# Kernel tuning notes

Hardware: AMD Instinct MI355X
Metric: run time of the kernel (lower is better)

The kernel has to match this reference:

```python
import jax, jax.numpy as jnp
import numpy as np

B, C, H_IMG, W_IMG = 16, 384, 56, 56
NUM_HEADS = 6
HEAD_DIM = C // NUM_HEADS
BN_EPS = 1e-5


def _bn(x, gamma, beta, mean, var):
    # x: [b, ch, n] or [b, ch, h, w]; per-channel affine normalization (eval-mode BatchNorm)
    shape = (1, -1) + (1,) * (x.ndim - 2)
    scale = (gamma / jnp.sqrt(var + BN_EPS)).reshape(shape)
    shift = (beta - mean * gamma / jnp.sqrt(var + BN_EPS)).reshape(shape)
    return x * scale + shift


def setup_inputs() -> dict:
    key = jax.random.key(0)
    ks = jax.random.split(key, 12)
    c2 = 2 * C
    return {
        "x": jax.random.normal(ks[0], (B, C, H_IMG, W_IMG), jnp.float32),
        "qk_w": jax.random.normal(ks[1], (c2, C // 2), jnp.float32) * 0.05,
        "qk_gamma": jax.random.uniform(ks[2], (c2,), jnp.float32, 0.5, 1.5),
        "qk_beta": jax.random.normal(ks[3], (c2,), jnp.float32) * 0.1,
        "qk_mean": jax.random.normal(ks[4], (c2,), jnp.float32) * 0.1,
        "qk_var": jax.random.uniform(ks[5], (c2,), jnp.float32, 0.5, 1.5),
        "pe_w": jax.random.normal(ks[6], (C, 1, 3, 3), jnp.float32) * 0.1,
        "pe_gamma": jax.random.uniform(ks[7], (C,), jnp.float32, 0.5, 1.5),
        "pe_beta": jax.random.normal(ks[8], (C,), jnp.float32) * 0.1,
        "pe_mean": jax.random.normal(ks[9], (C,), jnp.float32) * 0.1,
        "pe_var": jax.random.uniform(ks[10], (C,), jnp.float32, 0.5, 1.5),
    }


def reference(x, qk_w, qk_gamma, qk_beta, qk_mean, qk_var,
              pe_w, pe_gamma, pe_beta, pe_mean, pe_var):
    b, c, h, w = x.shape
    n = h * w
    s = n ** (-0.5)
    nh, hd = NUM_HEADS, HEAD_DIM

    # grouped (groups=2) 1x1 conv: out channels [0:c] from input [0:c/2], [c:2c] from [c/2:c]
    xg = x.reshape(b, 2, c // 2, n)                       # [b, 2, c/2, n]
    wg = qk_w.reshape(2, c, c // 2)                       # [group, out_per_group, in_per_group]
    qk = jnp.einsum('bgin,goi->bgon', xg, wg).reshape(b, 2 * c, n)
    qk = _bn(qk, qk_gamma, qk_beta, qk_mean, qk_var)
    qk = jax.nn.elu(qk) + 1.0

    qk = qk.reshape(b, 2, nh, hd, n)
    q, k = qk[:, 0], qk[:, 1]                             # [b, H, d, n]
    v = x.reshape(b, nh, hd, n)                           # [b, H, d, n]

    # kv = (k*s) @ (v^T * s): [b, H, d, d]
    kv = jnp.einsum('bhdn,bhen->bhde', k * s, v * s)
    # numerator: q^T @ kv -> [b, H, n, d]
    num = jnp.einsum('bhdn,bhde->bhne', q, kv)
    # denominator: q^T @ mean_n(k) -> [b, H, n]
    den = jnp.einsum('bhdn,bhd->bhn', q, k.mean(axis=-1)) + 1e-6
    attn = (num / den[..., None]).transpose(0, 1, 3, 2).reshape(b, c, h, w)

    # depthwise 3x3 conv positional encoding on v (= x) + BN
    pe = jax.lax.conv_general_dilated(
        x, pe_w, window_strides=(1, 1), padding=((1, 1), (1, 1)),
        feature_group_count=c, dimension_numbers=('NCHW', 'OIHW', 'NCHW'))
    pe = _bn(pe, pe_gamma, pe_beta, pe_mean, pe_var)

    return attn + pe
```

## Files before the change

### kernel.cpp

```cpp
#include <hip/hip_runtime.h>
#include <math.h>

#define N_SP 3136
#define BN_EPS 1e-5f

typedef __attribute__((ext_vector_type(8))) short short8;
typedef __attribute__((ext_vector_type(4))) float f32x4;

#define QK_SZ   (16*2*384*N_SP)
#define KVP_OFF (QK_SZ)
#define KVP_SZ  (16*6*7*64*80)
#define KV_OFF  (KVP_OFF + KVP_SZ)
#define KV_SZ   (16*6*64*64)
#define KM_OFF  (KV_OFF + KV_SZ)
#define KM_SZ   (16*6*64)
#define WH_OFF  (KM_OFF + KM_SZ)
#define WSPLIT_N (2*384*192)

__device__ __forceinline__ void bsplit(float f, ushort& h, ushort& l) {
    uint u = __float_as_uint(f);
    uint hr = (u + 0x7FFFu + ((u >> 16) & 1u)) >> 16;
    h = (ushort)hr;
    float fh = __uint_as_float(hr << 16);
    float fl = f - fh;
    uint v = __float_as_uint(fl);
    l = (ushort)((v + 0x7FFFu + ((v >> 16) & 1u)) >> 16);
}

__global__ __launch_bounds__(256) void p0_wsplit(
    const float* __restrict__ qk_w, ushort* __restrict__ wh, ushort* __restrict__ wl)
{
    int idx = blockIdx.x * 256 + threadIdx.x;
    if (idx >= WSPLIT_N) return;
    ushort h, l;
    bsplit(qk_w[idx], h, l);
    wh[idx] = h;
    wl[idx] = l;
}

__global__ __launch_bounds__(256) void k1_qk_mfma(
    const float* __restrict__ x, const ushort* __restrict__ wh, const ushort* __restrict__ wl,
    const float* __restrict__ gamma, const float* __restrict__ beta,
    const float* __restrict__ mean, const float* __restrict__ var,
    float* __restrict__ qk_out)
{
    __shared__ __align__(16) ushort Ah[8192];
    __shared__ __align__(16) ushort Al[8192];
    __shared__ __align__(16) ushort Bh[4096];
    __shared__ __align__(16) ushort Bl[4096];

    const int bx = blockIdx.x;
    const int by = blockIdx.y;
    const int bz = blockIdx.z;
    const int b = bz >> 1, gg = bz & 1;
    const int t = threadIdx.x;
    const int lane = t & 63, wv = t >> 6;
    const int wr = wv >> 1, wc = wv & 1;
    const int lg = lane >> 4, l15 = lane & 15;

    f32x4 acc[4][2];
    #pragma unroll
    for (int m = 0; m < 4; ++m)
        #pragma unroll
        for (int nf = 0; nf < 2; ++nf)
            acc[m][nf] = (f32x4){0.f, 0.f, 0.f, 0.f};

    const float* xg = x + (size_t)(b * 384 + gg * 192) * N_SP + bx * 64;
    const ushort* whg = wh + (gg * 384 + by * 128) * 192;
    const ushort* wlg = wl + (gg * 384 + by * 128) * 192;

    for (int kt = 0; kt < 3; ++kt) {
        #pragma unroll
        for (int li = 0; li < 4; ++li) {
            int c = li * 256 + t;
            int row = c >> 3, kb = c & 7;
            int goff = row * 192 + kt * 64 + kb * 8;
            float4 vh = *(const float4*)(whg + goff);
            float4 vl = *(const float4*)(wlg + goff);
            int ch = (row * 8 + (kb ^ (row & 7))) * 8;
            *(float4*)&Ah[ch] = vh;
            *(float4*)&Al[ch] = vl;
        }
        #pragma unroll
        for (int li = 0; li < 2; ++li) {
            int idx = li * 256 + t;
            int kp = idx >> 4;
            int nq = idx & 15;
            int k0 = kp * 2;
            const float* px = xg + (size_t)(kt * 64 + k0) * N_SP + nq * 4;
            float4 v0 = *(const float4*)px;
            float4 v1 = *(const float4*)(px + N_SP);
            ushort h0[4], l0[4], h1[4], l1[4];
            float a0[4] = {v0.x, v0.y, v0.z, v0.w};
            float a1[4] = {v1.x, v1.y, v1.z, v1.w};
            #pragma unroll
            for (int i = 0; i < 4; ++i) { bsplit(a0[i], h0[i], l0[i]); bsplit(a1[i], h1[i], l1[i]); }
            int kb = k0 >> 3, ks = (k0 & 6) >> 1;
            #pragma unroll
            for (int i = 0; i < 4; ++i) {
                int n = nq * 4 + i;
                int chunk = n * 8 + (kb ^ ((n >> 1) & 7));
                ((uint*)Bh)[chunk * 4 + ks] = (uint)h0[i] | ((uint)h1[i] << 16);
                ((uint*)Bl)[chunk * 4 + ks] = (uint)l0[i] | ((uint)l1[i] << 16);
            }
        }
        __syncthreads();
        #pragma unroll
        for (int s = 0; s < 2; ++s) {
            short8 ah[4], al[4], bh[2], bl[2];
            int kb = s * 4 + lg;
            #pragma unroll
            for (int m = 0; m < 4; ++m) {
                int row = wr * 64 + m * 16 + l15;
                int ch = (row * 8 + (kb ^ (row & 7))) * 8;
                ah[m] = *(const short8*)&Ah[ch];
                al[m] = *(const short8*)&Al[ch];
            }
            #pragma unroll
            for (int nf = 0; nf < 2; ++nf) {
                int n = wc * 32 + nf * 16 + l15;
                int ch = (n * 8 + (kb ^ ((n >> 1) & 7))) * 8;
                bh[nf] = *(const short8*)&Bh[ch];
                bl[nf] = *(const short8*)&Bl[ch];
            }
            #pragma unroll
            for (int m = 0; m < 4; ++m)
                #pragma unroll
                for (int nf = 0; nf < 2; ++nf) {
                    acc[m][nf] = __builtin_amdgcn_mfma_f32_16x16x32_bf16(ah[m], bh[nf], acc[m][nf], 0, 0, 0);
                    acc[m][nf] = __builtin_amdgcn_mfma_f32_16x16x32_bf16(ah[m], bl[nf], acc[m][nf], 0, 0, 0);
                    acc[m][nf] = __builtin_amdgcn_mfma_f32_16x16x32_bf16(al[m], bh[nf], acc[m][nf], 0, 0, 0);
                }
        }
        __syncthreads();
    }

    float* scs = (float*)Bh;
    float* shs = scs + 128;
    if (t < 128) {
        int ch = gg * 384 + by * 128 + t;
        float sc = gamma[ch] / sqrtf(var[ch] + BN_EPS);
        scs[t] = sc;
        shs[t] = beta[ch] - mean[ch] * sc;
    }
    __syncthreads();

    size_t obase = ((size_t)(b * 2 + gg) * 384 + by * 128) * N_SP + bx * 64 + wc * 32;
    #pragma unroll
    for (int m = 0; m < 4; ++m)
        #pragma unroll
        for (int nf = 0; nf < 2; ++nf) {
            #pragma unroll
            for (int r = 0; r < 4; ++r) {
                int orow = wr * 64 + m * 16 + lg * 4 + r;
                float v = acc[m][nf][r] * scs[orow] + shs[orow];
                v = v > 0.f ? v + 1.f : __expf(v);
                qk_out[obase + (size_t)orow * N_SP + nf * 16 + l15] = v;
            }
        }
}

__global__ __launch_bounds__(256) void k2_kv_mfma(
    const float* __restrict__ x, const float* __restrict__ qk,
    float* __restrict__ kv_part)
{
    __shared__ __align__(16) ushort Kh[4096], Kl[4096];
    __shared__ __align__(16) ushort Vh[5120], Vl[5120];

    const int chunk = blockIdx.x;
    const int h = blockIdx.y, b = blockIdx.z;
    const int t = threadIdx.x;
    const int lane = t & 63, wv = t >> 6;
    const int lg = lane >> 4, l15 = lane & 15;

    const float* kp = qk + (size_t)((b*2+1)*384 + h*64) * N_SP;
    const float* vp = x  + (size_t)(b*384 + h*64) * N_SP;

    #pragma unroll
    for (int li = 0; li < 4; ++li) {
        int idx = li * 256 + t;
        int row = 64 + (idx >> 6), col = idx & 63;
        int off = (row * 8 + ((col >> 3) ^ (row & 7))) * 8 + (col & 7);
        Vh[off] = (row == 64) ? (ushort)0x3F80 : (ushort)0;
        Vl[off] = 0;
    }

    f32x4 acc[5];
    #pragma unroll
    for (int nf = 0; nf < 5; ++nf) acc[nf] = (f32x4){0.f, 0.f, 0.f, 0.f};

    for (int sub = 0; sub < 7; ++sub) {
        int n0 = chunk * 448 + sub * 64;
        #pragma unroll
        for (int li = 0; li < 4; ++li) {
            int idx = li * 256 + t;
            int row = idx >> 4, sc = idx & 15;
            int off = (row * 8 + ((sc >> 1) ^ (row & 7))) * 8 + (sc & 1) * 4;
            float4 kf = *(const float4*)&kp[(size_t)row * N_SP + n0 + sc * 4];
            ushort h0,h1,h2,h3,l0,l1,l2,l3;
            bsplit(kf.x,h0,l0); bsplit(kf.y,h1,l1); bsplit(kf.z,h2,l2); bsplit(kf.w,h3,l3);
            ((uint*)&Kh[off])[0] = (uint)h0 | ((uint)h1 << 16);
            ((uint*)&Kh[off])[1] = (uint)h2 | ((uint)h3 << 16);
            ((uint*)&Kl[off])[0] = (uint)l0 | ((uint)l1 << 16);
            ((uint*)&Kl[off])[1] = (uint)l2 | ((uint)l3 << 16);
            float4 vf = *(const float4*)&vp[(size_t)row * N_SP + n0 + sc * 4];
            bsplit(vf.x,h0,l0); bsplit(vf.y,h1,l1); bsplit(vf.z,h2,l2); bsplit(vf.w,h3,l3);
            ((uint*)&Vh[off])[0] = (uint)h0 | ((uint)h1 << 16);
            ((uint*)&Vh[off])[1] = (uint)h2 | ((uint)h3 << 16);
            ((uint*)&Vl[off])[0] = (uint)l0 | ((uint)l1 << 16);
            ((uint*)&Vl[off])[1] = (uint)l2 | ((uint)l3 << 16);
        }
        __syncthreads();
        #pragma unroll
        for (int s = 0; s < 2; ++s) {
            int arow = wv * 16 + l15;
            int akb = (s * 4 + lg) ^ (arow & 7);
            short8 ah = *(const short8*)&Kh[(arow * 8 + akb) * 8];
            short8 al = *(const short8*)&Kl[(arow * 8 + akb) * 8];
            #pragma unroll
            for (int nf = 0; nf < 5; ++nf) {
                int brow = nf * 16 + l15;
                int bkb = (s * 4 + lg) ^ (brow & 7);
                short8 bh = *(const short8*)&Vh[(brow * 8 + bkb) * 8];
                short8 bl = *(const short8*)&Vl[(brow * 8 + bkb) * 8];
                acc[nf] = __builtin_amdgcn_mfma_f32_16x16x32_bf16(ah, bh, acc[nf], 0, 0, 0);
                acc[nf] = __builtin_amdgcn_mfma_f32_16x16x32_bf16(ah, bl, acc[nf], 0, 0, 0);
                acc[nf] = __builtin_amdgcn_mfma_f32_16x16x32_bf16(al, bh, acc[nf], 0, 0, 0);
            }
        }
        __syncthreads();
    }

    size_t base = (size_t)((b*6 + h)*7 + chunk) * 64 * 80;
    #pragma unroll
    for (int nf = 0; nf < 5; ++nf)
        #pragma unroll
        for (int r = 0; r < 4; ++r) {
            int d = wv * 16 + lg * 4 + r;
            kv_part[base + (size_t)d * 80 + nf * 16 + l15] = acc[nf][r];
        }
}

__global__ __launch_bounds__(256) void k2b_reduce(
    const float* __restrict__ kv_part,
    float* __restrict__ kv, float* __restrict__ km)
{
    int idx = blockIdx.x*256 + threadIdx.x;
    const float inv_n = 1.0f / (float)N_SP;
    if (idx < 16*6*64*64) {
        int bh = idx >> 12, de = idx & 4095;
        int d = de >> 6, e = de & 63;
        float s = 0.f;
        #pragma unroll
        for (int c = 0; c < 7; ++c) s += kv_part[((size_t)(bh*7+c)*64 + d)*80 + e];
        kv[idx] = s * inv_n;
    }
    if (idx < 16*6*64) {
        int bh = idx >> 6, d = idx & 63;
        float s = 0.f;
        #pragma unroll
        for (int c = 0; c < 7; ++c) s += kv_part[((size_t)(bh*7+c)*64 + d)*80 + 64];
        km[idx] = s * inv_n;
    }
}

__global__ __launch_bounds__(256) void k3_attn_pe(
    const float* __restrict__ x, const float* __restrict__ qk,
    const float* __restrict__ kv, const float* __restrict__ km,
    const float* __restrict__ pw,
    const float* __restrict__ pgamma, const float* __restrict__ pbeta,
    const float* __restrict__ pmean, const float* __restrict__ pvar,
    float* __restrict__ out)
{
    __shared__ float qs[64][68];
    __shared__ float kms[64];
    const int bx = blockIdx.x;
    const int h = blockIdx.y, b = blockIdx.z;
    const int t = threadIdx.x, tx = t & 15, ty = t >> 4;
    const int n0 = bx*64;
    const float* qp  = qk + (size_t)((b*2+0)*384 + h*64)*N_SP;
    const float* kvp = kv + (b*6+h)*4096;
    #pragma unroll
    for (int l = 0; l < 4; ++l) {
        int idx = t + l*256;
        int d = idx >> 4, c = idx & 15;
        *(float4*)&qs[d][c*4] = *(const float4*)&qp[(size_t)d*N_SP + n0 + c*4];
    }
    if (t < 64) kms[t] = km[(b*6+h)*64 + t];
    __syncthreads();

    float acc[4][4] = {};
    float den[4] = {};
    #pragma unroll 8
    for (int d = 0; d < 64; ++d) {
        float4 qn = *(const float4*)&qs[d][tx*4];
        float4 ke = *(const float4*)&kvp[d*64 + ty*4];
        float qq[4] = {qn.x,qn.y,qn.z,qn.w}, kk[4] = {ke.x,ke.y,ke.z,ke.w};
        float kmd = kms[d];
        #pragma unroll
        for (int p = 0; p < 4; ++p) {
            den[p] += qq[p]*kmd;
            #pragma unroll
            for (int j = 0; j < 4; ++j) acc[p][j] += qq[p]*kk[j];
        }
    }

    const int p0 = n0 + tx*4;
    const int y = p0 / 56, xc = p0 % 56;
    #pragma unroll
    for (int j = 0; j < 4; ++j) {
        int c = h*64 + ty*4 + j;
        const float* xp = x + ((size_t)b*384 + c)*N_SP;
        float s6[3][6];
        #pragma unroll
        for (int dy = 0; dy < 3; ++dy) {
            int yy = y + dy - 1;
            bool yok = (yy >= 0) && (yy < 56);
            float4 mid = make_float4(0.f,0.f,0.f,0.f);
            float lf = 0.f, rt = 0.f;
            if (yok) {
                const float* xr = xp + yy*56;
                mid = *(const float4*)&xr[xc];
                if (xc > 0)  lf = xr[xc-1];
                if (xc < 52) rt = xr[xc+4];
            }
            s6[dy][0]=lf; s6[dy][1]=mid.x; s6[dy][2]=mid.y;
            s6[dy][3]=mid.z; s6[dy][4]=mid.w; s6[dy][5]=rt;
        }
        float w9[9];
        #pragma unroll
        for (int q = 0; q < 9; ++q) w9[q] = pw[c*9 + q];
        float sc2 = pgamma[c] / sqrtf(pvar[c] + BN_EPS);
        float sh2 = pbeta[c] - pmean[c]*sc2;
        float4 r;
        float* pr = (float*)&r;
        #pragma unroll
        for (int p = 0; p < 4; ++p) {
            float conv = 0.f;
            #pragma unroll
            for (int dy = 0; dy < 3; ++dy)
                #pragma unroll
                for (int dx = 0; dx < 3; ++dx)
                    conv += w9[dy*3+dx] * s6[dy][p + dx];
            pr[p] = acc[p][j] / (den[p] + 1e-6f) + (conv*sc2 + sh2);
        }
        *(float4*)&out[((size_t)b*384 + c)*N_SP + p0] = r;
    }
}

extern "C" void kernel_launch(void* const* d_in, const int* in_sizes, int n_in,
                              void* d_out, int out_size, void* d_ws, size_t ws_size,
                              hipStream_t stream)
{
    const float* x        = (const float*)d_in[0];
    const float* qk_w     = (const float*)d_in[1];
    const float* qk_gamma = (const float*)d_in[2];
    const float* qk_beta  = (const float*)d_in[3];
    const float* qk_mean  = (const float*)d_in[4];
    const float* qk_var   = (const float*)d_in[5];
    const float* pe_w     = (const float*)d_in[6];
    const float* pe_gamma = (const float*)d_in[7];
    const float* pe_beta  = (const float*)d_in[8];
    const float* pe_mean  = (const float*)d_in[9];
    const float* pe_var   = (const float*)d_in[10];
    float* out = (float*)d_out;

    float* ws      = (float*)d_ws;
    float* qk      = ws;
    float* kv_part = ws + KVP_OFF;
    float* kv      = ws + KV_OFF;
    float* km      = ws + KM_OFF;
    ushort* whp    = (ushort*)(ws + WH_OFF);
    ushort* wlp    = whp + WSPLIT_N;

    hipLaunchKernelGGL(p0_wsplit, dim3((WSPLIT_N + 255)/256), dim3(256), 0, stream,
                       qk_w, whp, wlp);
    dim3 g1(49, 3, 32);
    hipLaunchKernelGGL(k1_qk_mfma, g1, dim3(256), 0, stream,
                       x, whp, wlp, qk_gamma, qk_beta, qk_mean, qk_var, qk);
    dim3 g2(7, 6, 16);
    hipLaunchKernelGGL(k2_kv_mfma, g2, dim3(256), 0, stream, x, qk, kv_part);
    hipLaunchKernelGGL(k2b_reduce, dim3(1536), dim3(256), 0, stream,
                       kv_part, kv, km);
    dim3 g3(49, 6, 16);
    hipLaunchKernelGGL(k3_attn_pe, g3, dim3(256), 0, stream,
                       x, qk, kv, km, pe_w, pe_gamma, pe_beta, pe_mean, pe_var, out);
}
```

Before: 219.8 us.

## Compute attention numerator and denominator in k3 via split-bf16 MFMA

The reduce kernel now emits kv and the k-mean row, transposed and split into bf16 high/low halves, padded to 80 rows. The attention kernel converts its q tile to split bf16 in swizzled shared memory. It then computes numerator and denominator with three-pass MFMA instead of scalar FMAs, staging the results through shared memory for the PE epilogue. This cuts the per-block FP32 FMA work in k3, at the cost of extra conversion, shared memory traffic, two more barriers, and slight precision change from bf16x3 emulation.

```diff
diff --git a/kernel.cpp b/kernel.cpp
--- a/kernel.cpp
+++ b/kernel.cpp
@@ -10,11 +10,9 @@
 #define QK_SZ   (16*2*384*N_SP)
 #define KVP_OFF (QK_SZ)
 #define KVP_SZ  (16*6*7*64*80)
-#define KV_OFF  (KVP_OFF + KVP_SZ)
-#define KV_SZ   (16*6*64*64)
-#define KM_OFF  (KV_OFF + KV_SZ)
-#define KM_SZ   (16*6*64)
-#define WH_OFF  (KM_OFF + KM_SZ)
+#define KVT_OFF (KVP_OFF + KVP_SZ)
+#define KVT_FSZ (2*96*80*64/2)
+#define WH_OFF  (KVT_OFF + KVT_FSZ)
 #define WSPLIT_N (2*384*192)
 
 __device__ __forceinline__ void bsplit(float f, ushort& h, ushort& l) {
@@ -243,95 +241,146 @@
 
 __global__ __launch_bounds__(256) void k2b_reduce(
     const float* __restrict__ kv_part,
-    float* __restrict__ kv, float* __restrict__ km)
-{
-    int idx = blockIdx.x*256 + threadIdx.x;
+    ushort* __restrict__ kvt_h, ushort* __restrict__ kvt_l)
+{
+    const int bh = blockIdx.x;
+    const int t = threadIdx.x;
     const float inv_n = 1.0f / (float)N_SP;
-    if (idx < 16*6*64*64) {
-        int bh = idx >> 12, de = idx & 4095;
-        int d = de >> 6, e = de & 63;
+    const float* base = kv_part + (size_t)bh * 7 * 64 * 80;
+    ushort* oh = kvt_h + (size_t)bh * 80 * 64;
+    ushort* ol = kvt_l + (size_t)bh * 80 * 64;
+    for (int i = t; i < 80 * 64; i += 256) {
+        int e = i >> 6, d = i & 63;
         float s = 0.f;
-        #pragma unroll
-        for (int c = 0; c < 7; ++c) s += kv_part[((size_t)(bh*7+c)*64 + d)*80 + e];
-        kv[idx] = s * inv_n;
-    }
-    if (idx < 16*6*64) {
-        int bh = idx >> 6, d = idx & 63;
-        float s = 0.f;
-        #pragma unroll
-        for (int c = 0; c < 7; ++c) s += kv_part[((size_t)(bh*7+c)*64 + d)*80 + 64];
-        km[idx] = s * inv_n;
-    }
-}
-
+        if (e <= 64) {
+            #pragma unroll
+            for (int c = 0; c < 7; ++c) s += base[(size_t)(c * 64 + d) * 80 + e];
+            s *= inv_n;
+        }
+        ushort h, l;
+        bsplit(s, h, l);
+        oh[i] = h; ol[i] = l;
+    }
+}
+
+#define ATT_STRIDE 68
 __global__ __launch_bounds__(256) void k3_attn_pe(
     const float* __restrict__ x, const float* __restrict__ qk,
-    const float* __restrict__ kv, const float* __restrict__ km,
+    const ushort* __restrict__ kvt_h, const ushort* __restrict__ kvt_l,
     const float* __restrict__ pw,
     const float* __restrict__ pgamma, const float* __restrict__ pbeta,
     const float* __restrict__ pmean, const float* __restrict__ pvar,
     float* __restrict__ out)
 {
-    __shared__ float qs[64][68];
-    __shared__ float kms[64];
+    __shared__ __align__(16) float SBF[ATT_STRIDE * 64 + 64];
+    ushort* Qh = (ushort*)SBF;
+    ushort* Ql = Qh + 4096;
+
     const int bx = blockIdx.x;
     const int h = blockIdx.y, b = blockIdx.z;
-    const int t = threadIdx.x, tx = t & 15, ty = t >> 4;
-    const int n0 = bx*64;
-    const float* qp  = qk + (size_t)((b*2+0)*384 + h*64)*N_SP;
-    const float* kvp = kv + (b*6+h)*4096;
-    #pragma unroll
-    for (int l = 0; l < 4; ++l) {
-        int idx = t + l*256;
-        int d = idx >> 4, c = idx & 15;
-        *(float4*)&qs[d][c*4] = *(const float4*)&qp[(size_t)d*N_SP + n0 + c*4];
-    }
-    if (t < 64) kms[t] = km[(b*6+h)*64 + t];
+    const int t = threadIdx.x;
+    const int lane = t & 63, wv = t >> 6;
+    const int lg = lane >> 4, l15 = lane & 15;
+    const int n0 = bx * 64;
+    const float* qp = qk + (size_t)((b*2+0)*384 + h*64) * N_SP + n0;
+
+    #pragma unroll
+    for (int li = 0; li < 2; ++li) {
+        int idx = li * 256 + t;
+        int kp2 = idx >> 4;
+        int nq = idx & 15;
+        int k0 = kp2 * 2;
+        const float* px = qp + (size_t)k0 * N_SP + nq * 4;
+        float4 v0 = *(const float4*)px;
+        float4 v1 = *(const float4*)(px + N_SP);
+        ushort h0[4], l0[4], h1[4], l1[4];
+        float a0[4] = {v0.x, v0.y, v0.z, v0.w};
+        float a1[4] = {v1.x, v1.y, v1.z, v1.w};
+        #pragma unroll
+        for (int i = 0; i < 4; ++i) { bsplit(a0[i], h0[i], l0[i]); bsplit(a1[i], h1[i], l1[i]); }
+        int kb = k0 >> 3, ks = (k0 & 6) >> 1;
+        #pragma unroll
+        for (int i = 0; i < 4; ++i) {
+            int n = nq * 4 + i;
+            int chunk = n * 8 + (kb ^ ((n >> 1) & 7));
+            ((uint*)Qh)[chunk * 4 + ks] = (uint)h0[i] | ((uint)h1[i] << 16);
+            ((uint*)Ql)[chunk * 4 + ks] = (uint)l0[i] | ((uint)l1[i] << 16);
+        }
+    }
     __syncthreads();
 
-    float acc[4][4] = {};
-    float den[4] = {};
-    #pragma unroll 8
-    for (int d = 0; d < 64; ++d) {
-        float4 qn = *(const float4*)&qs[d][tx*4];
-        float4 ke = *(const float4*)&kvp[d*64 + ty*4];
-        float qq[4] = {qn.x,qn.y,qn.z,qn.w}, kk[4] = {ke.x,ke.y,ke.z,ke.w};
-        float kmd = kms[d];
-        #pragma unroll
-        for (int p = 0; p < 4; ++p) {
-            den[p] += qq[p]*kmd;
-            #pragma unroll
-            for (int j = 0; j < 4; ++j) acc[p][j] += qq[p]*kk[j];
-        }
-    }
-
-    const int p0 = n0 + tx*4;
+    short8 bqh[2], bql[2];
+    #pragma unroll
+    for (int s = 0; s < 2; ++s) {
+        int n = wv * 16 + l15;
+        int chunk = n * 8 + ((s * 4 + lg) ^ ((n >> 1) & 7));
+        bqh[s] = *(const short8*)&Qh[chunk * 8];
+        bql[s] = *(const short8*)&Ql[chunk * 8];
+    }
+    __syncthreads();
+
+    const ushort* ahb = kvt_h + (size_t)(b*6 + h) * 80 * 64;
+    const ushort* alb = kvt_l + (size_t)(b*6 + h) * 80 * 64;
+    f32x4 acc[5];
+    #pragma unroll
+    for (int m = 0; m < 5; ++m) acc[m] = (f32x4){0.f, 0.f, 0.f, 0.f};
+    #pragma unroll
+    for (int s = 0; s < 2; ++s) {
+        #pragma unroll
+        for (int m = 0; m < 5; ++m) {
+            int off = (m * 16 + l15) * 64 + (s * 4 + lg) * 8;
+            short8 ah = *(const short8*)&ahb[off];
+            short8 al = *(const short8*)&alb[off];
+            acc[m] = __builtin_amdgcn_mfma_f32_16x16x32_bf16(ah, bqh[s], acc[m], 0, 0, 0);
+            acc[m] = __builtin_amdgcn_mfma_f32_16x16x32_bf16(ah, bql[s], acc[m], 0, 0, 0);
+            acc[m] = __builtin_amdgcn_mfma_f32_16x16x32_bf16(al, bqh[s], acc[m], 0, 0, 0);
+        }
+    }
+
+    {
+        int ncol = wv * 16 + l15;
+        #pragma unroll
+        for (int m = 0; m < 4; ++m)
+            #pragma unroll
+            for (int r = 0; r < 4; ++r)
+                SBF[(m * 16 + lg * 4 + r) * ATT_STRIDE + ncol] = acc[m][r];
+        if (lg == 0)
+            SBF[ATT_STRIDE * 64 + ncol] = acc[4][0];
+    }
+    __syncthreads();
+
+    const int tx = t & 15, ty = t >> 4;
+    const int p0 = n0 + tx * 4;
     const int y = p0 / 56, xc = p0 % 56;
+    float den[4];
+    #pragma unroll
+    for (int p = 0; p < 4; ++p) den[p] = SBF[ATT_STRIDE * 64 + tx * 4 + p] + 1e-6f;
     #pragma unroll
     for (int j = 0; j < 4; ++j) {
-        int c = h*64 + ty*4 + j;
-        const float* xp = x + ((size_t)b*384 + c)*N_SP;
+        int cc = ty * 4 + j;
+        int c = h * 64 + cc;
+        const float* xp = x + ((size_t)b * 384 + c) * N_SP;
         float s6[3][6];
         #pragma unroll
         for (int dy = 0; dy < 3; ++dy) {
             int yy = y + dy - 1;
             bool yok = (yy >= 0) && (yy < 56);
-            float4 mid = make_float4(0.f,0.f,0.f,0.f);
+            float4 mid = make_float4(0.f, 0.f, 0.f, 0.f);
             float lf = 0.f, rt = 0.f;
             if (yok) {
-                const float* xr = xp + yy*56;
+                const float* xr = xp + yy * 56;
                 mid = *(const float4*)&xr[xc];
-                if (xc > 0)  lf = xr[xc-1];
-                if (xc < 52) rt = xr[xc+4];
-            }
-            s6[dy][0]=lf; s6[dy][1]=mid.x; s6[dy][2]=mid.y;
-            s6[dy][3]=mid.z; s6[dy][4]=mid.w; s6[dy][5]=rt;
+                if (xc > 0)  lf = xr[xc - 1];
+                if (xc < 52) rt = xr[xc + 4];
+            }
+            s6[dy][0] = lf;  s6[dy][1] = mid.x; s6[dy][2] = mid.y;
+            s6[dy][3] = mid.z; s6[dy][4] = mid.w; s6[dy][5] = rt;
         }
         float w9[9];
         #pragma unroll
-        for (int q = 0; q < 9; ++q) w9[q] = pw[c*9 + q];
+        for (int q = 0; q < 9; ++q) w9[q] = pw[c * 9 + q];
         float sc2 = pgamma[c] / sqrtf(pvar[c] + BN_EPS);
-        float sh2 = pbeta[c] - pmean[c]*sc2;
+        float sh2 = pbeta[c] - pmean[c] * sc2;
         float4 r;
         float* pr = (float*)&r;
         #pragma unroll
@@ -341,10 +390,11 @@
             for (int dy = 0; dy < 3; ++dy)
                 #pragma unroll
                 for (int dx = 0; dx < 3; ++dx)
-                    conv += w9[dy*3+dx] * s6[dy][p + dx];
-            pr[p] = acc[p][j] / (den[p] + 1e-6f) + (conv*sc2 + sh2);
-        }
-        *(float4*)&out[((size_t)b*384 + c)*N_SP + p0] = r;
+                    conv += w9[dy * 3 + dx] * s6[dy][p + dx];
+            float num = SBF[cc * ATT_STRIDE + tx * 4 + p];
+            pr[p] = num / den[p] + (conv * sc2 + sh2);
+        }
+        *(float4*)&out[((size_t)b * 384 + c) * N_SP + p0] = r;
     }
 }
 
@@ -368,8 +418,8 @@
     float* ws      = (float*)d_ws;
     float* qk      = ws;
     float* kv_part = ws + KVP_OFF;
-    float* kv      = ws + KV_OFF;
-    float* km      = ws + KM_OFF;
+    ushort* kvt_h  = (ushort*)(ws + KVT_OFF);
+    ushort* kvt_l  = kvt_h + 96 * 80 * 64;
     ushort* whp    = (ushort*)(ws + WH_OFF);
     ushort* wlp    = whp + WSPLIT_N;
 
@@ -380,9 +430,9 @@
                        x, whp, wlp, qk_gamma, qk_beta, qk_mean, qk_var, qk);
     dim3 g2(7, 6, 16);
     hipLaunchKernelGGL(k2_kv_mfma, g2, dim3(256), 0, stream, x, qk, kv_part);
-    hipLaunchKernelGGL(k2b_reduce, dim3(1536), dim3(256), 0, stream,
-                       kv_part, kv, km);
+    hipLaunchKernelGGL(k2b_reduce, dim3(96), dim3(256), 0, stream,
+                       kv_part, kvt_h, kvt_l);
     dim3 g3(49, 6, 16);
     hipLaunchKernelGGL(k3_attn_pe, g3, dim3(256), 0, stream,
-                       x, qk, kv, km, pe_w, pe_gamma, pe_beta, pe_mean, pe_var, out);
-}
+                       x, qk, kvt_h, kvt_l, pe_w, pe_gamma, pe_beta, pe_mean, pe_var, out);
+}
```

Measured after the change: 240.5 us. +9.4%, slower.

## Pre-split K to bf16 pairs, fold PE BN into weights, restructure attention kernel

Applied to the files above, without the earlier changes.

In k1 the K half is now stored as packed bf16 hi/lo pairs, so k2 no longer re-splits K; Q is written to its own fp32 buffer. The PE BatchNorm scale is folded into the depthwise weights in the prep kernel. The kv reduction is reorganised per (b,h) block. The final kernel maps one pixel per lane and 16 channels per wave, reading q straight from global memory instead of staging it in LDS, and does the 3x3 conv with scalar loads. The LDS swizzle for B in k1 also changes. The new conv path issues more scattered scalar loads of x, and the attention loop relies on the cache for q reuse.

```diff
diff --git a/kernel.cpp b/kernel.cpp
--- a/kernel.cpp
+++ b/kernel.cpp
@@ -7,15 +7,21 @@
 typedef __attribute__((ext_vector_type(8))) short short8;
 typedef __attribute__((ext_vector_type(4))) float f32x4;
 
-#define QK_SZ   (16*2*384*N_SP)
-#define KVP_OFF (QK_SZ)
+#define K_SZ    (16*384*N_SP)
+#define QB_OFF  (K_SZ)
+#define QB_SZ   (16*384*N_SP)
+#define KVP_OFF (QB_OFF + QB_SZ)
 #define KVP_SZ  (16*6*7*64*80)
-#define KV_OFF  (KVP_OFF + KVP_SZ)
-#define KV_SZ   (16*6*64*64)
-#define KM_OFF  (KV_OFF + KV_SZ)
+#define KVF_OFF (KVP_OFF + KVP_SZ)
+#define KVF_SZ  (16*6*64*64)
+#define KM_OFF  (KVF_OFF + KVF_SZ)
 #define KM_SZ   (16*6*64)
 #define WH_OFF  (KM_OFF + KM_SZ)
 #define WSPLIT_N (2*384*192)
+#define PWS_OFF (WH_OFF + WSPLIT_N)
+#define PSH_OFF (PWS_OFF + 384*9)
+
+#define FSWZ(n) ((((n) >> 1) ^ ((n) >> 2)) & 7)
 
 __device__ __forceinline__ void bsplit(float f, ushort& h, ushort& l) {
     uint u = __float_as_uint(f);
@@ -27,22 +33,33 @@
     l = (ushort)((v + 0x7FFFu + ((v >> 16) & 1u)) >> 16);
 }
 
-__global__ __launch_bounds__(256) void p0_wsplit(
-    const float* __restrict__ qk_w, ushort* __restrict__ wh, ushort* __restrict__ wl)
+__global__ __launch_bounds__(256) void p0_prep(
+    const float* __restrict__ qk_w, const float* __restrict__ pe_w,
+    const float* __restrict__ pgamma, const float* __restrict__ pbeta,
+    const float* __restrict__ pmean, const float* __restrict__ pvar,
+    ushort* __restrict__ wh, ushort* __restrict__ wl,
+    float* __restrict__ pwsc, float* __restrict__ psh)
 {
     int idx = blockIdx.x * 256 + threadIdx.x;
-    if (idx >= WSPLIT_N) return;
-    ushort h, l;
-    bsplit(qk_w[idx], h, l);
-    wh[idx] = h;
-    wl[idx] = l;
+    if (idx < WSPLIT_N) {
+        ushort h, l;
+        bsplit(qk_w[idx], h, l);
+        wh[idx] = h;
+        wl[idx] = l;
+    }
+    if (idx < 384) {
+        float sc = pgamma[idx] / sqrtf(pvar[idx] + BN_EPS);
+        psh[idx] = pbeta[idx] - pmean[idx] * sc;
+        #pragma unroll
+        for (int q = 0; q < 9; ++q) pwsc[idx * 9 + q] = pe_w[idx * 9 + q] * sc;
+    }
 }
 
 __global__ __launch_bounds__(256) void k1_qk_mfma(
     const float* __restrict__ x, const ushort* __restrict__ wh, const ushort* __restrict__ wl,
     const float* __restrict__ gamma, const float* __restrict__ beta,
     const float* __restrict__ mean, const float* __restrict__ var,
-    float* __restrict__ qk_out)
+    uint* __restrict__ kq, float* __restrict__ qbuf)
 {
     __shared__ __align__(16) ushort Ah[8192];
     __shared__ __align__(16) ushort Al[8192];
@@ -99,7 +116,7 @@
             #pragma unroll
             for (int i = 0; i < 4; ++i) {
                 int n = nq * 4 + i;
-                int chunk = n * 8 + (kb ^ ((n >> 1) & 7));
+                int chunk = n * 8 + (kb ^ FSWZ(n));
                 ((uint*)Bh)[chunk * 4 + ks] = (uint)h0[i] | ((uint)h1[i] << 16);
                 ((uint*)Bl)[chunk * 4 + ks] = (uint)l0[i] | ((uint)l1[i] << 16);
             }
@@ -119,7 +136,7 @@
             #pragma unroll
             for (int nf = 0; nf < 2; ++nf) {
                 int n = wc * 32 + nf * 16 + l15;
-                int ch = (n * 8 + (kb ^ ((n >> 1) & 7))) * 8;
+                int ch = (n * 8 + (kb ^ FSWZ(n))) * 8;
                 bh[nf] = *(const short8*)&Bh[ch];
                 bl[nf] = *(const short8*)&Bl[ch];
             }
@@ -145,23 +162,40 @@
     }
     __syncthreads();
 
-    size_t obase = ((size_t)(b * 2 + gg) * 384 + by * 128) * N_SP + bx * 64 + wc * 32;
-    #pragma unroll
-    for (int m = 0; m < 4; ++m)
-        #pragma unroll
-        for (int nf = 0; nf < 2; ++nf) {
-            #pragma unroll
-            for (int r = 0; r < 4; ++r) {
-                int orow = wr * 64 + m * 16 + lg * 4 + r;
-                float v = acc[m][nf][r] * scs[orow] + shs[orow];
-                v = v > 0.f ? v + 1.f : __expf(v);
-                qk_out[obase + (size_t)orow * N_SP + nf * 16 + l15] = v;
-            }
-        }
+    size_t obase = ((size_t)b * 384 + by * 128) * N_SP + bx * 64 + wc * 32;
+    if (gg == 0) {
+        #pragma unroll
+        for (int m = 0; m < 4; ++m)
+            #pragma unroll
+            for (int nf = 0; nf < 2; ++nf) {
+                #pragma unroll
+                for (int r = 0; r < 4; ++r) {
+                    int orow = wr * 64 + m * 16 + lg * 4 + r;
+                    float v = acc[m][nf][r] * scs[orow] + shs[orow];
+                    v = v > 0.f ? v + 1.f : __expf(v);
+                    qbuf[obase + (size_t)orow * N_SP + nf * 16 + l15] = v;
+                }
+            }
+    } else {
+        #pragma unroll
+        for (int m = 0; m < 4; ++m)
+            #pragma unroll
+            for (int nf = 0; nf < 2; ++nf) {
+                #pragma unroll
+                for (int r = 0; r < 4; ++r) {
+                    int orow = wr * 64 + m * 16 + lg * 4 + r;
+                    float v = acc[m][nf][r] * scs[orow] + shs[orow];
+                    v = v > 0.f ? v + 1.f : __expf(v);
+                    ushort hh, ll;
+                    bsplit(v, hh, ll);
+                    kq[obase + (size_t)orow * N_SP + nf * 16 + l15] = (uint)hh | ((uint)ll << 16);
+                }
+            }
+    }
 }
 
 __global__ __launch_bounds__(256) void k2_kv_mfma(
-    const float* __restrict__ x, const float* __restrict__ qk,
+    const float* __restrict__ x, const uint* __restrict__ kq,
     float* __restrict__ kv_part)
 {
     __shared__ __align__(16) ushort Kh[4096], Kl[4096];
@@ -173,7 +207,7 @@
     const int lane = t & 63, wv = t >> 6;
     const int lg = lane >> 4, l15 = lane & 15;
 
-    const float* kp = qk + (size_t)((b*2+1)*384 + h*64) * N_SP;
+    const uint* kp  = kq + (size_t)(b*384 + h*64) * N_SP;
     const float* vp = x  + (size_t)(b*384 + h*64) * N_SP;
 
     #pragma unroll
@@ -196,14 +230,13 @@
             int idx = li * 256 + t;
             int row = idx >> 4, sc = idx & 15;
             int off = (row * 8 + ((sc >> 1) ^ (row & 7))) * 8 + (sc & 1) * 4;
-            float4 kf = *(const float4*)&kp[(size_t)row * N_SP + n0 + sc * 4];
+            uint4 kf = *(const uint4*)&kp[(size_t)row * N_SP + n0 + sc * 4];
+            ((uint*)&Kh[off])[0] = (kf.x & 0xFFFFu) | (kf.y << 16);
+            ((uint*)&Kh[off])[1] = (kf.z & 0xFFFFu) | (kf.w << 16);
+            ((uint*)&Kl[off])[0] = (kf.x >> 16) | (kf.y & 0xFFFF0000u);
+            ((uint*)&Kl[off])[1] = (kf.z >> 16) | (kf.w & 0xFFFF0000u);
+            float4 vf = *(const float4*)&vp[(size_t)row * N_SP + n0 + sc * 4];
             ushort h0,h1,h2,h3,l0,l1,l2,l3;
-            bsplit(kf.x,h0,l0); bsplit(kf.y,h1,l1); bsplit(kf.z,h2,l2); bsplit(kf.w,h3,l3);
-            ((uint*)&Kh[off])[0] = (uint)h0 | ((uint)h1 << 16);
-            ((uint*)&Kh[off])[1] = (uint)h2 | ((uint)h3 << 16);
-            ((uint*)&Kl[off])[0] = (uint)l0 | ((uint)l1 << 16);
-            ((uint*)&Kl[off])[1] = (uint)l2 | ((uint)l3 << 16);
-            float4 vf = *(const float4*)&vp[(size_t)row * N_SP + n0 + sc * 4];
             bsplit(vf.x,h0,l0); bsplit(vf.y,h1,l1); bsplit(vf.z,h2,l2); bsplit(vf.w,h3,l3);
             ((uint*)&Vh[off])[0] = (uint)h0 | ((uint)h1 << 16);
             ((uint*)&Vh[off])[1] = (uint)h2 | ((uint)h3 << 16);
@@ -243,108 +276,87 @@
 
 __global__ __launch_bounds__(256) void k2b_reduce(
     const float* __restrict__ kv_part,
-    float* __restrict__ kv, float* __restrict__ km)
-{
-    int idx = blockIdx.x*256 + threadIdx.x;
+    float* __restrict__ kvf, float* __restrict__ km)
+{
+    const int bh = blockIdx.x;
+    const int t = threadIdx.x;
     const float inv_n = 1.0f / (float)N_SP;
-    if (idx < 16*6*64*64) {
-        int bh = idx >> 12, de = idx & 4095;
-        int d = de >> 6, e = de & 63;
-        float s = 0.f;
-        #pragma unroll
-        for (int c = 0; c < 7; ++c) s += kv_part[((size_t)(bh*7+c)*64 + d)*80 + e];
-        kv[idx] = s * inv_n;
-    }
-    if (idx < 16*6*64) {
-        int bh = idx >> 6, d = idx & 63;
-        float s = 0.f;
-        #pragma unroll
-        for (int c = 0; c < 7; ++c) s += kv_part[((size_t)(bh*7+c)*64 + d)*80 + 64];
-        km[idx] = s * inv_n;
-    }
-}
-
-__global__ __launch_bounds__(256) void k3_attn_pe(
-    const float* __restrict__ x, const float* __restrict__ qk,
-    const float* __restrict__ kv, const float* __restrict__ km,
-    const float* __restrict__ pw,
-    const float* __restrict__ pgamma, const float* __restrict__ pbeta,
-    const float* __restrict__ pmean, const float* __restrict__ pvar,
+    const float* base = kv_part + (size_t)bh * 7 * 5120;
+    float s[20];
+    #pragma unroll
+    for (int j = 0; j < 20; ++j) s[j] = 0.f;
+    for (int c = 0; c < 7; ++c) {
+        #pragma unroll
+        for (int j = 0; j < 20; ++j) s[j] += base[c * 5120 + j * 256 + t];
+    }
+    #pragma unroll
+    for (int j = 0; j < 20; ++j) {
+        int i = j * 256 + t;
+        int d = i / 80, e = i % 80;
+        float v = s[j] * inv_n;
+        if (e < 64)       kvf[(size_t)bh * 4096 + d * 64 + e] = v;
+        else if (e == 64) km[bh * 64 + d] = v;
+    }
+}
+
+__global__ __launch_bounds__(256) void k3_stream(
+    const float* __restrict__ qbuf, const float* __restrict__ kvf,
+    const float* __restrict__ km, const float* __restrict__ x,
+    const float* __restrict__ pwsc, const float* __restrict__ psh,
     float* __restrict__ out)
 {
-    __shared__ float qs[64][68];
-    __shared__ float kms[64];
     const int bx = blockIdx.x;
     const int h = blockIdx.y, b = blockIdx.z;
-    const int t = threadIdx.x, tx = t & 15, ty = t >> 4;
-    const int n0 = bx*64;
-    const float* qp  = qk + (size_t)((b*2+0)*384 + h*64)*N_SP;
-    const float* kvp = kv + (b*6+h)*4096;
-    #pragma unroll
-    for (int l = 0; l < 4; ++l) {
-        int idx = t + l*256;
-        int d = idx >> 4, c = idx & 15;
-        *(float4*)&qs[d][c*4] = *(const float4*)&qp[(size_t)d*N_SP + n0 + c*4];
-    }
-    if (t < 64) kms[t] = km[(b*6+h)*64 + t];
-    __syncthreads();
-
-    float acc[4][4] = {};
-    float den[4] = {};
-    #pragma unroll 8
+    const int t = threadIdx.x;
+    const int lam = t & 63;
+    const int w = t >> 6;
+    const int n = bx * 64 + lam;
+    const int ebase = w * 16;
+
+    const float* qp  = qbuf + (size_t)(b * 384 + h * 64) * N_SP + n;
+    const float* kvp = kvf + (size_t)(b * 6 + h) * 4096 + ebase;
+    const float* kmp = km + (b * 6 + h) * 64;
+
+    float acc[16];
+    #pragma unroll
+    for (int e = 0; e < 16; ++e) acc[e] = 0.f;
+    float den = 0.f;
+
+    #pragma unroll 4
     for (int d = 0; d < 64; ++d) {
-        float4 qn = *(const float4*)&qs[d][tx*4];
-        float4 ke = *(const float4*)&kvp[d*64 + ty*4];
-        float qq[4] = {qn.x,qn.y,qn.z,qn.w}, kk[4] = {ke.x,ke.y,ke.z,ke.w};
-        float kmd = kms[d];
-        #pragma unroll
-        for (int p = 0; p < 4; ++p) {
-            den[p] += qq[p]*kmd;
-            #pragma unroll
-            for (int j = 0; j < 4; ++j) acc[p][j] += qq[p]*kk[j];
-        }
-    }
-
-    const int p0 = n0 + tx*4;
-    const int y = p0 / 56, xc = p0 % 56;
-    #pragma unroll
-    for (int j = 0; j < 4; ++j) {
-        int c = h*64 + ty*4 + j;
-        const float* xp = x + ((size_t)b*384 + c)*N_SP;
-        float s6[3][6];
+        float qd = qp[(size_t)d * N_SP];
+        den += qd * kmp[d];
+        const float* kr = kvp + d * 64;
+        #pragma unroll
+        for (int eq = 0; eq < 4; ++eq) {
+            float4 k4 = *(const float4*)(kr + eq * 4);
+            acc[eq * 4 + 0] += qd * k4.x;
+            acc[eq * 4 + 1] += qd * k4.y;
+            acc[eq * 4 + 2] += qd * k4.z;
+            acc[eq * 4 + 3] += qd * k4.w;
+        }
+    }
+    const float r = 1.0f / (den + 1e-6f);
+
+    const int y = n / 56, xc = n % 56;
+    const bool xlo = (xc > 0), xhi = (xc < 55);
+    #pragma unroll
+    for (int e = 0; e < 16; ++e) {
+        int c = h * 64 + ebase + e;
+        const float* xp = x + ((size_t)b * 384 + c) * N_SP;
+        const float* wp = pwsc + c * 9;
+        float conv = 0.f;
         #pragma unroll
         for (int dy = 0; dy < 3; ++dy) {
             int yy = y + dy - 1;
             bool yok = (yy >= 0) && (yy < 56);
-            float4 mid = make_float4(0.f,0.f,0.f,0.f);
-            float lf = 0.f, rt = 0.f;
-            if (yok) {
-                const float* xr = xp + yy*56;
-                mid = *(const float4*)&xr[xc];
-                if (xc > 0)  lf = xr[xc-1];
-                if (xc < 52) rt = xr[xc+4];
-            }
-            s6[dy][0]=lf; s6[dy][1]=mid.x; s6[dy][2]=mid.y;
-            s6[dy][3]=mid.z; s6[dy][4]=mid.w; s6[dy][5]=rt;
-        }
-        float w9[9];
-        #pragma unroll
-        for (int q = 0; q < 9; ++q) w9[q] = pw[c*9 + q];
-        float sc2 = pgamma[c] / sqrtf(pvar[c] + BN_EPS);
-        float sh2 = pbeta[c] - pmean[c]*sc2;
-        float4 r;
-        float* pr = (float*)&r;
-        #pragma unroll
-        for (int p = 0; p < 4; ++p) {
-            float conv = 0.f;
-            #pragma unroll
-            for (int dy = 0; dy < 3; ++dy)
-                #pragma unroll
-                for (int dx = 0; dx < 3; ++dx)
-                    conv += w9[dy*3+dx] * s6[dy][p + dx];
-            pr[p] = acc[p][j] / (den[p] + 1e-6f) + (conv*sc2 + sh2);
-        }
-        *(float4*)&out[((size_t)b*384 + c)*N_SP + p0] = r;
+            const float* xr = xp + yy * 56 + xc;
+            float t0 = (yok && xlo) ? xr[-1] : 0.f;
+            float t1 = yok ? xr[0] : 0.f;
+            float t2 = (yok && xhi) ? xr[1] : 0.f;
+            conv += wp[dy * 3 + 0] * t0 + wp[dy * 3 + 1] * t1 + wp[dy * 3 + 2] * t2;
+        }
+        out[((size_t)b * 384 + c) * N_SP + n] = acc[e] * r + conv + psh[c];
     }
 }
 
@@ -366,23 +378,27 @@
     float* out = (float*)d_out;
 
     float* ws      = (float*)d_ws;
-    float* qk      = ws;
+    uint* kq       = (uint*)ws;
+    float* qbuf    = ws + QB_OFF;
     float* kv_part = ws + KVP_OFF;
-    float* kv      = ws + KV_OFF;
+    float* kvf     = ws + KVF_OFF;
     float* km      = ws + KM_OFF;
     ushort* whp    = (ushort*)(ws + WH_OFF);
     ushort* wlp    = whp + WSPLIT_N;
-
-    hipLaunchKernelGGL(p0_wsplit, dim3((WSPLIT_N + 255)/256), dim3(256), 0, stream,
-                       qk_w, whp, wlp);
+    float* pwsc    = ws + PWS_OFF;
+    float* psh     = ws + PSH_OFF;
+
+    hipLaunchKernelGGL(p0_prep, dim3((WSPLIT_N + 255)/256), dim3(256), 0, stream,
+                       qk_w, pe_w, pe_gamma, pe_beta, pe_mean, pe_var,
+                       whp, wlp, pwsc, psh);
     dim3 g1(49, 3, 32);
     hipLaunchKernelGGL(k1_qk_mfma, g1, dim3(256), 0, stream,
-                       x, whp, wlp, qk_gamma, qk_beta, qk_mean, qk_var, qk);
+                       x, whp, wlp, qk_gamma, qk_beta, qk_mean, qk_var, kq, qbuf);
     dim3 g2(7, 6, 16);
-    hipLaunchKernelGGL(k2_kv_mfma, g2, dim3(256), 0, stream, x, qk, kv_part);
-    hipLaunchKernelGGL(k2b_reduce, dim3(1536), dim3(256), 0, stream,
-                       kv_part, kv, km);
+    hipLaunchKernelGGL(k2_kv_mfma, g2, dim3(256), 0, stream, x, kq, kv_part);
+    hipLaunchKernelGGL(k2b_reduce, dim3(96), dim3(256), 0, stream,
+                       kv_part, kvf, km);
     dim3 g3(49, 6, 16);
-    hipLaunchKernelGGL(k3_attn_pe, g3, dim3(256), 0, stream,
-                       x, qk, kv, km, pe_w, pe_gamma, pe_beta, pe_mean, pe_var, out);
-}
+    hipLaunchKernelGGL(k3_stream, g3, dim3(256), 0, stream,
+                       qbuf, kvf, km, x, pwsc, psh, out);
+}
```

Result: slower. 325.0 us (+47.8%).
